# Kernel optimization log

Measured on AMD Instinct MI355X. Metric: run time of the kernel, lower is better.

Reference implementation:

```python
import jax, jax.numpy as jnp
import numpy as np

D_MODEL = 2048
NUM_HEADS = 16
HEAD_DIM = D_MODEL // NUM_HEADS
B, T = 2, 2048


def setup_inputs() -> dict:
    key = jax.random.key(0)
    ks = jax.random.split(key, 6)
    x = jax.random.normal(ks[0], (B, T, D_MODEL), dtype=jnp.float32)
    # RoPE tables: angles theta_i = 10000^(-2i/d), half-dim tables [T, HEAD_DIM//2]
    pos = jnp.arange(T, dtype=jnp.float32)[:, None]
    inv_freq = 1.0 / (10000.0 ** (jnp.arange(0, HEAD_DIM, 2, dtype=jnp.float32) / HEAD_DIM))
    ang = pos * inv_freq[None, :]
    sin = jnp.sin(ang)
    cos = jnp.cos(ang)
    doc_ids = jnp.sort(jax.random.randint(ks[1], (B, T), 0, 4), axis=-1).astype(jnp.int32)
    W_qkv = jax.random.normal(ks[2], (D_MODEL, D_MODEL + 2 * HEAD_DIM), dtype=jnp.float32) * 0.02
    W_out = jax.random.normal(ks[3], (D_MODEL, D_MODEL), dtype=jnp.float32) * 0.02
    return {"x": x, "sin": sin, "cos": cos, "doc_ids": doc_ids, "W_qkv": W_qkv, "W_out": W_out}


def _apply_rope(x, sin, cos):
    # x: [..., T, ..., HEAD_DIM]; sin/cos: [T, HEAD_DIM//2], broadcast to x's rank
    if x.ndim == 4:  # [B, T, H, D]
        s, c = sin[None, :, None, :], cos[None, :, None, :]
    else:  # [B, T, D]
        s, c = sin[None, :, :], cos[None, :, :]
    x1, x2 = jnp.split(x, 2, axis=-1)
    return jnp.concatenate([x1 * c - x2 * s, x2 * c + x1 * s], axis=-1)


def reference(x, sin, cos, doc_ids, W_qkv, W_out):
    b, t, _ = x.shape
    qkv = x @ W_qkv  # [B, T, D_MODEL + 2*HEAD_DIM]
    q = qkv[..., :D_MODEL].reshape(b, t, NUM_HEADS, HEAD_DIM)
    k = qkv[..., D_MODEL:D_MODEL + HEAD_DIM]  # [B, T, HEAD_DIM] single KV head
    v = qkv[..., D_MODEL + HEAD_DIM:]         # [B, T, HEAD_DIM]
    q = _apply_rope(q, sin, cos)
    k = _apply_rope(k, sin, cos)
    # doc-packed causal mask -> additive bias [B, 1, T, T]
    neg_inf = jnp.finfo(q.dtype).min / 2
    causal = jnp.tril(jnp.ones((t, t), dtype=jnp.bool_))
    same_doc = doc_ids[:, :, None] == doc_ids[:, None, :]
    mask = (causal[None, :, :] & same_doc)[:, None, :, :]
    bias = jnp.where(mask, jnp.array(0.0, q.dtype), neg_inf)
    scale = 1.0 / jnp.sqrt(jnp.array(HEAD_DIM, q.dtype))
    scores = jnp.einsum("bthd,bsd->bhts", q, k) * scale + bias  # [B, H, T, T]
    attn = jax.nn.softmax(scores, axis=-1)
    out = jnp.einsum("bhts,bsd->bthd", attn, v).reshape(b, t, D_MODEL)
    return out @ W_out
```

## Files before the change

kernel.cpp:

```cpp
#include <hip/hip_runtime.h>
#include <math.h>

#define D_MODEL 2048
#define NUM_HEADS 16
#define HEAD_DIM 128
#define BB 2
#define TT 2048
#define QKV_N 2304
#define KOFF 2048
#define VOFF 2176

typedef __attribute__((ext_vector_type(8))) short short8;
typedef __attribute__((ext_vector_type(4))) float f32x4;

static __device__ __forceinline__ short f2bf(float f) {
  union { float f; unsigned u; } x; x.f = f;
  unsigned r = (x.u + 0x7FFFu + ((x.u >> 16) & 1u)) >> 16;
  return (short)r;
}
static __device__ __forceinline__ float bf2f(unsigned short u) {
  return __uint_as_float(((unsigned)u) << 16);
}

#define GLD16(gp, lp)                                              \
  __builtin_amdgcn_global_load_lds(                                \
      (const __attribute__((address_space(1))) void*)(gp),         \
      (__attribute__((address_space(3))) void*)(lp), 16, 0, 0)

static __device__ __forceinline__ void swizzle_xy(int& bx, int& by) {
  const int gx = gridDim.x;
  const int lin = blockIdx.y * gx + blockIdx.x;
  const int band = lin / (gx * 8);
  const int rem = lin - band * gx * 8;
  by = band * 8 + (rem & 7);
  bx = rem >> 3;
}

__global__ __launch_bounds__(256) void gemm_qkv_rope(
    const short* __restrict__ A, const short* __restrict__ Bt,
    short* __restrict__ qkv, short* __restrict__ Vtb,
    const float* __restrict__ sin_t, const float* __restrict__ cos_t)
{
  __shared__ short As[2][128 * 32];
  __shared__ short Bs[2][128 * 32];
  const int K = D_MODEL;

  int bx, by;
  swizzle_xy(bx, by);

  const int tid = threadIdx.x;
  const int w = tid >> 6, l = tid & 63;
  const int quad = l >> 4, l16 = l & 15;
  const int wm = w >> 1, wn = w & 1;
  const int m0 = by * 128, n0 = bx * 128;

  f32x4 acc[4][4];
#pragma unroll
  for (int i = 0; i < 4; i++)
#pragma unroll
    for (int j = 0; j < 4; j++) acc[i][j] = (f32x4){0.f, 0.f, 0.f, 0.f};

  const int cswz = ((l & 3) ^ ((l >> 3) & 3)) * 8;
  const short* aA = A + (size_t)(m0 + w * 32 + (l >> 2)) * K + cswz;
  const short* aB = Bt + (size_t)(n0 + w * 32 + (l >> 2)) * K + cswz;
  const int lwo = w * 1024;

  const int aswz = (quad ^ ((l16 >> 1) & 3)) * 8;
  const short* Ard = &As[0][0] + (size_t)(wm * 64 + l16) * 32 + aswz;
  const short* Brd = &Bs[0][0] + (size_t)(wn * 16 + l16) * 32 + aswz;

  auto stage = [&](int buf, int go) {
    short* la = &As[buf][0] + lwo;
    short* lb = &Bs[buf][0] + lwo;
    GLD16(aA + go, la);
    GLD16(aA + go + (size_t)16 * K, la + 512);
    GLD16(aB + go, lb);
    GLD16(aB + go + (size_t)16 * K, lb + 512);
  };

  auto compute = [&](int buf) {
    const short* Ac = Ard + buf * 4096;
    const short* Bc = Brd + buf * 4096;
    short8 af[4], bf[4];
#pragma unroll
    for (int mi = 0; mi < 4; mi++)
      af[mi] = *(const short8*)(Ac + mi * 512);
#pragma unroll
    for (int ni = 0; ni < 4; ni++)
      bf[ni] = *(const short8*)(Bc + ni * 1024);
#pragma unroll
    for (int mi = 0; mi < 4; mi++)
#pragma unroll
      for (int ni = 0; ni < 4; ni++)
        acc[mi][ni] =
            __builtin_amdgcn_mfma_f32_16x16x32_bf16(af[mi], bf[ni], acc[mi][ni], 0, 0, 0);
  };

  stage(0, 0);
  __syncthreads();
  int cur = 0;
#pragma unroll 2
  for (int k0 = 32; k0 < K; k0 += 32) {
    stage(cur ^ 1, k0);
    compute(cur);
    __syncthreads();
    cur ^= 1;
  }
  compute(cur);

  const int colbase = wn * 16 + l16;
  const bool is_v = (n0 == VOFF);

#pragma unroll
  for (int mi = 0; mi < 4; mi++) {
#pragma unroll
    for (int r = 0; r < 4; r++) {
      const int row = m0 + wm * 64 + mi * 16 + quad * 4 + r;
      const int b = row >> 11, t = row & (TT - 1);
#pragma unroll
      for (int ni = 0; ni < 2; ni++) {
        const int cloc = ni * 32 + colbase;
        const float c1 = acc[mi][ni][r];
        const float c2 = acc[mi][ni + 2][r];
        if (!is_v) {
          const float sn = sin_t[t * 64 + cloc];
          const float cs = cos_t[t * 64 + cloc];
          short* op = qkv + (size_t)row * QKV_N + n0 + cloc;
          op[0]  = f2bf(c1 * cs - c2 * sn);
          op[64] = f2bf(c2 * cs + c1 * sn);
        } else {
          Vtb[((size_t)(b * 128 + cloc) << 11) + t]      = f2bf(c1);
          Vtb[((size_t)(b * 128 + cloc + 64) << 11) + t] = f2bf(c2);
        }
      }
    }
  }
}

__global__ __launch_bounds__(256) void gemm_mfma_bt(
    const short* __restrict__ A, const short* __restrict__ Bt,
    float* __restrict__ C, int M, int N, int K)
{
  __shared__ short As[2][128 * 32];
  __shared__ short Bs[2][128 * 32];

  int bx, by;
  swizzle_xy(bx, by);

  const int tid = threadIdx.x;
  const int w = tid >> 6, l = tid & 63;
  const int quad = l >> 4, l16 = l & 15;
  const int wm = w >> 1, wn = w & 1;
  const int m0 = by * 128, n0 = bx * 128;

  f32x4 acc[4][4];
#pragma unroll
  for (int i = 0; i < 4; i++)
#pragma unroll
    for (int j = 0; j < 4; j++) acc[i][j] = (f32x4){0.f, 0.f, 0.f, 0.f};

  const int cswz = ((l & 3) ^ ((l >> 3) & 3)) * 8;
  const short* aA = A + (size_t)(m0 + w * 32 + (l >> 2)) * K + cswz;
  const short* aB = Bt + (size_t)(n0 + w * 32 + (l >> 2)) * K + cswz;
  const int lwo = w * 1024;

  const int aswz = (quad ^ ((l16 >> 1) & 3)) * 8;
  const short* Ard = &As[0][0] + (size_t)(wm * 64 + l16) * 32 + aswz;
  const short* Brd = &Bs[0][0] + (size_t)(wn * 64 + l16) * 32 + aswz;

  auto stage = [&](int buf, int go) {
    short* la = &As[buf][0] + lwo;
    short* lb = &Bs[buf][0] + lwo;
    GLD16(aA + go, la);
    GLD16(aA + go + (size_t)16 * K, la + 512);
    GLD16(aB + go, lb);
    GLD16(aB + go + (size_t)16 * K, lb + 512);
  };

  auto compute = [&](int buf) {
    const short* Ac = Ard + buf * 4096;
    const short* Bc = Brd + buf * 4096;
    short8 af[4], bf[4];
#pragma unroll
    for (int mi = 0; mi < 4; mi++)
      af[mi] = *(const short8*)(Ac + mi * 512);
#pragma unroll
    for (int ni = 0; ni < 4; ni++)
      bf[ni] = *(const short8*)(Bc + ni * 512);
#pragma unroll
    for (int mi = 0; mi < 4; mi++)
#pragma unroll
      for (int ni = 0; ni < 4; ni++)
        acc[mi][ni] =
            __builtin_amdgcn_mfma_f32_16x16x32_bf16(af[mi], bf[ni], acc[mi][ni], 0, 0, 0);
  };

  stage(0, 0);
  __syncthreads();
  int cur = 0;
#pragma unroll 2
  for (int k0 = 32; k0 < K; k0 += 32) {
    stage(cur ^ 1, k0);
    compute(cur);
    __syncthreads();
    cur ^= 1;
  }
  compute(cur);

#pragma unroll
  for (int mi = 0; mi < 4; mi++) {
#pragma unroll
    for (int ni = 0; ni < 4; ni++) {
#pragma unroll
      for (int r = 0; r < 4; r++) {
        const int row = m0 + wm * 64 + mi * 16 + quad * 4 + r;
        const int col = n0 + wn * 64 + ni * 16 + l16;
        C[(size_t)row * N + col] = acc[mi][ni][r];
      }
    }
  }
}

#define XB_BLOCKS 8192
#define WQ_BLOCKS (72 * 64)
#define WO_BLOCKS (64 * 64)

__global__ __launch_bounds__(256) void prep_all(
    const float* __restrict__ x, short* __restrict__ xb,
    const float* __restrict__ Wq, short* __restrict__ Wqt,
    const float* __restrict__ Wo, short* __restrict__ Wot)
{
  const int bid = blockIdx.x;
  const int tid = threadIdx.x;

  if (bid < XB_BLOCKS) {
    const size_t i4 = (size_t)bid * 256 + tid;
    float4 v = *(const float4*)(x + i4 * 4);
    short4 o;
    o.x = f2bf(v.x); o.y = f2bf(v.y); o.z = f2bf(v.z); o.w = f2bf(v.w);
    *(short4*)(xb + i4 * 4) = o;
    return;
  }

  __shared__ float t[32][33];
  const float* W;
  short* Wt;
  int N, tile, ntx;
  if (bid < XB_BLOCKS + WQ_BLOCKS) {
    tile = bid - XB_BLOCKS; W = Wq; Wt = Wqt; N = QKV_N; ntx = 72;
  } else {
    tile = bid - XB_BLOCKS - WQ_BLOCKS; W = Wo; Wt = Wot; N = D_MODEL; ntx = 64;
  }
  const int K = D_MODEL;
  const int bx = tile % ntx, byy = tile / ntx;
  const int tx = tid & 31, ty = tid >> 5;
  const int n0 = bx * 32, k0 = byy * 32;
#pragma unroll
  for (int j = 0; j < 4; j++)
    t[ty + j * 8][tx] = W[(size_t)(k0 + ty + j * 8) * N + n0 + tx];
  __syncthreads();
#pragma unroll
  for (int j = 0; j < 4; j++)
    Wt[(size_t)(n0 + ty + j * 8) * K + k0 + tx] = f2bf(t[tx][ty + j * 8]);
}

#define KSTR 136
#define VSTR 72
#define PSTR 72

__global__ __launch_bounds__(256) void attn_mfma(
    const short* __restrict__ qkv, const short* __restrict__ Vtb,
    const int* __restrict__ doc_ids, short* __restrict__ attn_out)
{
  __shared__ short Ks[64 * KSTR];
  __shared__ short Vt[128 * VSTR];
  __shared__ short Pbuf[4 * 16 * PSTR];
  __shared__ int doc_s[64];

  const int qt = blockIdx.x, h = blockIdx.y, b = blockIdx.z;
  const int q0 = qt * 64;
  const int tid = threadIdx.x;
  const int w = tid >> 6;
  const int lane = tid & 63;
  const int quad = lane >> 4, l16 = lane & 15;

  const short* qp = qkv + (size_t)(b * TT + q0 + w * 16 + l16) * QKV_N
                    + h * HEAD_DIM + quad * 8;
  short8 Qf[4];
#pragma unroll
  for (int kc = 0; kc < 4; kc++) Qf[kc] = *(const short8*)(qp + kc * 32);

  const int docmin_q = doc_ids[b * TT + q0];
  const int docmax_q = doc_ids[b * TT + q0 + 63];

  int qg[4], mydoc[4];
  float l_i[4];
#pragma unroll
  for (int r = 0; r < 4; r++) {
    qg[r] = q0 + w * 16 + quad * 4 + r;
    mydoc[r] = doc_ids[b * TT + qg[r]];
    l_i[r] = 0.f;
  }
  f32x4 O[8];
#pragma unroll
  for (int v8 = 0; v8 < 8; v8++) O[v8] = (f32x4){0.f, 0.f, 0.f, 0.f};

  short* Pw = Pbuf + w * 16 * PSTR;
  const float scale = 0.08838834764831844f;

  for (int st = 0; st <= qt; st++) {
    const int s0 = st * 64;
    const int dmin_s = doc_ids[b * TT + s0];
    const int dmax_s = doc_ids[b * TT + s0 + 63];
    if (dmax_s < docmin_q) continue;
    const bool full = (st < qt) && (dmin_s == docmax_q);

    __syncthreads();
#pragma unroll
    for (int i = 0; i < 4; i++) {
      int f = i * 256 + tid;
      int row = f >> 4, seg = f & 15;
      int4 v = *(const int4*)(qkv + (size_t)(b * TT + s0 + row) * QKV_N + KOFF + seg * 8);
      *(int4*)(Ks + row * KSTR + seg * 8) = v;
    }
#pragma unroll
    for (int i = 0; i < 4; i++) {
      int f = i * 256 + tid;
      int n = f >> 3, seg = f & 7;
      int4 v = *(const int4*)(Vtb + ((size_t)(b * 128 + n) << 11) + s0 + seg * 8);
      *(int4*)(Vt + n * VSTR + seg * 8) = v;
    }
    if (!full && tid < 64) doc_s[tid] = doc_ids[b * TT + s0 + tid];
    __syncthreads();

    f32x4 S[4];
#pragma unroll
    for (int ns = 0; ns < 4; ns++) {
      f32x4 acc = (f32x4){0.f, 0.f, 0.f, 0.f};
      const short* kr = Ks + (ns * 16 + l16) * KSTR + quad * 8;
#pragma unroll
      for (int kc = 0; kc < 4; kc++) {
        short8 kf = *(const short8*)(kr + kc * 32);
        acc = __builtin_amdgcn_mfma_f32_16x16x32_bf16(Qf[kc], kf, acc, 0, 0, 0);
      }
      S[ns] = acc;
    }

    if (full) {
#pragma unroll
      for (int ns = 0; ns < 4; ns++)
#pragma unroll
        for (int r = 0; r < 4; r++) {
          const float p = __expf(S[ns][r] * scale);
          l_i[r] += p;
          Pw[(quad * 4 + r) * PSTR + ns * 16 + l16] = f2bf(p);
        }
    } else {
#pragma unroll
      for (int ns = 0; ns < 4; ns++) {
        const int s_loc = ns * 16 + l16;
        const int sg = s0 + s_loc;
        const int sdoc = doc_s[s_loc];
#pragma unroll
        for (int r = 0; r < 4; r++) {
          const bool ok = (sg <= qg[r]) && (sdoc == mydoc[r]);
          const float p = ok ? __expf(S[ns][r] * scale) : 0.f;
          l_i[r] += p;
          Pw[(quad * 4 + r) * PSTR + ns * 16 + l16] = f2bf(p);
        }
      }
    }

#pragma unroll
    for (int ks = 0; ks < 2; ks++) {
      short8 pf = *(const short8*)(Pw + l16 * PSTR + ks * 32 + quad * 8);
#pragma unroll
      for (int v8 = 0; v8 < 8; v8++) {
        short8 vf = *(const short8*)(Vt + (v8 * 16 + l16) * VSTR + ks * 32 + quad * 8);
        O[v8] = __builtin_amdgcn_mfma_f32_16x16x32_bf16(pf, vf, O[v8], 0, 0, 0);
      }
    }
  }

#pragma unroll
  for (int off = 8; off >= 1; off >>= 1)
#pragma unroll
    for (int r = 0; r < 4; r++) l_i[r] += __shfl_xor(l_i[r], off);

#pragma unroll
  for (int r = 0; r < 4; r++) {
    const float inv = 1.f / l_i[r];
    short* op = attn_out + (size_t)(b * TT + qg[r]) * D_MODEL + h * HEAD_DIM + l16;
#pragma unroll
    for (int v8 = 0; v8 < 8; v8++)
      op[v8 * 16] = f2bf(O[v8][r] * inv);
  }
}

extern "C" void kernel_launch(void* const* d_in, const int* in_sizes, int n_in,
                              void* d_out, int out_size, void* d_ws, size_t ws_size,
                              hipStream_t stream)
{
  const float* x     = (const float*)d_in[0];
  const float* sin_t = (const float*)d_in[1];
  const float* cos_t = (const float*)d_in[2];
  const int*   doc   = (const int*)  d_in[3];
  const float* W_qkv = (const float*)d_in[4];
  const float* W_out = (const float*)d_in[5];
  float* out = (float*)d_out;

  const int M = BB * TT;

  char* p = (char*)d_ws;
  short* qkv_bf = (short*)p; p += (size_t)M * QKV_N * 2;
  short* xb     = (short*)p; p += (size_t)M * D_MODEL * 2;
  short* attn_bf = xb;
  short* Vtb    = (short*)p; p += (size_t)BB * 128 * TT * 2;
  short* Wqkv_t = (short*)p; p += (size_t)QKV_N * D_MODEL * 2;
  short* Wout_t = (short*)p;

  prep_all<<<XB_BLOCKS + WQ_BLOCKS + WO_BLOCKS, 256, 0, stream>>>(
      x, xb, W_qkv, Wqkv_t, W_out, Wout_t);

  {
    dim3 grid(QKV_N / 128, M / 128);
    gemm_qkv_rope<<<grid, 256, 0, stream>>>(xb, Wqkv_t, qkv_bf, Vtb, sin_t, cos_t);
  }
  {
    dim3 grid(TT / 64, NUM_HEADS, BB);
    attn_mfma<<<grid, 256, 0, stream>>>(qkv_bf, Vtb, doc, attn_bf);
  }
  {
    dim3 grid(D_MODEL / 128, M / 128);
    gemm_mfma_bt<<<grid, 256, 0, stream>>>(attn_bf, Wout_t, out, M, D_MODEL, D_MODEL);
  }
}
```

Before: 286.2 us.

## Triple-buffer LDS in both GEMMs with a two-stage-ahead prefetch

Both bf16 MFMA GEMM kernels move from double to triple LDS buffering and prefetch two K-slices ahead using global_load_lds. The full __syncthreads is replaced by an explicit s_waitcnt vmcnt(4) plus s_barrier, so one stage of loads can stay in flight across each barrier. The aim is to hide global-memory latency behind MFMA work. The cost is 1.5x the LDS use, which may lower occupancy, and the vmcnt(4) value silently assumes each stage issues exactly four loads per thread.

Result: no change. 285.6 us (-0.2%).

```diff
diff --git a/kernel.cpp b/kernel.cpp
--- a/kernel.cpp
+++ b/kernel.cpp
@@ -41,8 +41,8 @@
     short* __restrict__ qkv, short* __restrict__ Vtb,
     const float* __restrict__ sin_t, const float* __restrict__ cos_t)
 {
-  __shared__ short As[2][128 * 32];
-  __shared__ short Bs[2][128 * 32];
+  __shared__ short As[3][128 * 32];
+  __shared__ short Bs[3][128 * 32];
   const int K = D_MODEL;
 
   int bx, by;
@@ -96,17 +96,28 @@
             __builtin_amdgcn_mfma_f32_16x16x32_bf16(af[mi], bf[ni], acc[mi][ni], 0, 0, 0);
   };
 
+  const int NI = K / 32;
   stage(0, 0);
-  __syncthreads();
+  stage(1, 32);
+  asm volatile("s_waitcnt vmcnt(4)" ::: "memory");
+  __builtin_amdgcn_s_barrier();
+
   int cur = 0;
-#pragma unroll 2
-  for (int k0 = 32; k0 < K; k0 += 32) {
-    stage(cur ^ 1, k0);
+  for (int i = 0; i < NI; ++i) {
+    if (i + 2 < NI) {
+      int bs = cur + 2; if (bs >= 3) bs -= 3;
+      stage(bs, (i + 2) * 32);
+    }
     compute(cur);
-    __syncthreads();
-    cur ^= 1;
-  }
-  compute(cur);
+    if (i + 1 < NI) {
+      if (i + 2 < NI)
+        asm volatile("s_waitcnt vmcnt(4)" ::: "memory");
+      else
+        asm volatile("s_waitcnt vmcnt(0)" ::: "memory");
+      __builtin_amdgcn_s_barrier();
+    }
+    cur = (cur + 1 == 3) ? 0 : cur + 1;
+  }
 
   const int colbase = wn * 16 + l16;
   const bool is_v = (n0 == VOFF);
@@ -141,8 +152,8 @@
     const short* __restrict__ A, const short* __restrict__ Bt,
     float* __restrict__ C, int M, int N, int K)
 {
-  __shared__ short As[2][128 * 32];
-  __shared__ short Bs[2][128 * 32];
+  __shared__ short As[3][128 * 32];
+  __shared__ short Bs[3][128 * 32];
 
   int bx, by;
   swizzle_xy(bx, by);
@@ -195,17 +206,28 @@
             __builtin_amdgcn_mfma_f32_16x16x32_bf16(af[mi], bf[ni], acc[mi][ni], 0, 0, 0);
   };
 
+  const int NI = K / 32;
   stage(0, 0);
-  __syncthreads();
+  stage(1, 32);
+  asm volatile("s_waitcnt vmcnt(4)" ::: "memory");
+  __builtin_amdgcn_s_barrier();
+
   int cur = 0;
-#pragma unroll 2
-  for (int k0 = 32; k0 < K; k0 += 32) {
-    stage(cur ^ 1, k0);
+  for (int i = 0; i < NI; ++i) {
+    if (i + 2 < NI) {
+      int bs = cur + 2; if (bs >= 3) bs -= 3;
+      stage(bs, (i + 2) * 32);
+    }
     compute(cur);
-    __syncthreads();
-    cur ^= 1;
-  }
-  compute(cur);
+    if (i + 1 < NI) {
+      if (i + 2 < NI)
+        asm volatile("s_waitcnt vmcnt(4)" ::: "memory");
+      else
+        asm volatile("s_waitcnt vmcnt(0)" ::: "memory");
+      __builtin_amdgcn_s_barrier();
+    }
+    cur = (cur + 1 == 3) ? 0 : cur + 1;
+  }
 
 #pragma unroll
   for (int mi = 0; mi < 4; mi++) {
```
